# Performance work log

Hardware: AMD Instinct MI355X
Metric: run time of the kernel (lower is better)

Reference implementation:

```python
import jax, jax.numpy as jnp
import numpy as np

N, E, G = 50000, 800000, 64
IN_CH, HID, HEADS, NUM_CLASSES = 128, 64, 4, 10
NEG_SLOPE = 0.2


def _gat_conv(x, src, dst, W, a_src, a_dst, b, concat):
    """PyG-style GATConv with default add_self_loops=True (inference mode)."""
    n = x.shape[0]
    H, C = a_src.shape
    h = (x @ W).reshape(n, H, C)                       # [N,H,C]
    loop = jnp.arange(n, dtype=src.dtype)
    si = jnp.concatenate([src, loop])                  # [E+N]
    di = jnp.concatenate([dst, loop])
    as_n = jnp.sum(h * a_src, axis=-1)                 # [N,H]
    ad_n = jnp.sum(h * a_dst, axis=-1)                 # [N,H]
    e = jax.nn.leaky_relu(as_n[si] + ad_n[di], NEG_SLOPE)   # [E+N,H]
    m = jax.ops.segment_max(e, di, num_segments=n)     # segment softmax (stable)
    ex = jnp.exp(e - m[di])
    denom = jax.ops.segment_sum(ex, di, num_segments=n)
    alpha = ex / (denom[di] + 1e-16)                   # [E+N,H]
    out = jax.ops.segment_sum(alpha[:, :, None] * h[si], di, num_segments=n)  # [N,H,C]
    out = out.reshape(n, H * C) if concat else out.mean(axis=1)
    return out + b


def setup_inputs() -> dict:
    key = jax.random.key(0)
    ks = jax.random.split(key, 20)
    d = {}
    d["x"] = jax.random.normal(ks[0], (N, IN_CH), dtype=jnp.float32)
    d["src"] = jax.random.randint(ks[1], (E,), 0, N, dtype=jnp.int32)
    d["dst"] = jax.random.randint(ks[2], (E,), 0, N, dtype=jnp.int32)
    d["batch"] = jnp.sort(jax.random.randint(ks[3], (N,), 0, G, dtype=jnp.int32))
    s = 0.1
    d["W1"] = jax.random.normal(ks[4], (IN_CH, HEADS * HID), dtype=jnp.float32) * s
    d["as1"] = jax.random.normal(ks[5], (HEADS, HID), dtype=jnp.float32) * s
    d["ad1"] = jax.random.normal(ks[6], (HEADS, HID), dtype=jnp.float32) * s
    d["b1"] = jnp.zeros((HEADS * HID,), jnp.float32)
    d["W2"] = jax.random.normal(ks[7], (HEADS * HID, HEADS * HID), dtype=jnp.float32) * s
    d["as2"] = jax.random.normal(ks[8], (HEADS, HID), dtype=jnp.float32) * s
    d["ad2"] = jax.random.normal(ks[9], (HEADS, HID), dtype=jnp.float32) * s
    d["b2"] = jnp.zeros((HEADS * HID,), jnp.float32)
    # proj: 256 -> 64, heads=1, concat=False
    d["Wp"] = jax.random.normal(ks[10], (HEADS * HID, HID), dtype=jnp.float32) * s
    d["asp"] = jax.random.normal(ks[11], (1, HID), dtype=jnp.float32) * s
    d["adp"] = jax.random.normal(ks[12], (1, HID), dtype=jnp.float32) * s
    d["bp"] = jnp.zeros((HID,), jnp.float32)
    # MLP head
    d["Wh1"] = jax.random.normal(ks[13], (HID, HID), dtype=jnp.float32) * s
    d["bh1"] = jnp.zeros((HID,), jnp.float32)
    d["Wh2"] = jax.random.normal(ks[14], (HID, NUM_CLASSES), dtype=jnp.float32) * s
    d["bh2"] = jnp.zeros((NUM_CLASSES,), jnp.float32)
    return d


def reference(x, src, dst, batch, W1, as1, ad1, b1, W2, as2, ad2, b2,
              Wp, asp, adp, bp, Wh1, bh1, Wh2, bh2):
    h = jax.nn.elu(_gat_conv(x, src, dst, W1, as1, ad1, b1, concat=True))
    h = jax.nn.elu(_gat_conv(h, src, dst, W2, as2, ad2, b2, concat=True))
    h = jax.nn.elu(_gat_conv(h, src, dst, Wp, asp, adp, bp, concat=False))  # [N,HID]
    # global mean pool over graphs
    sums = jax.ops.segment_sum(h, batch, num_segments=G)                    # [G,HID]
    cnt = jax.ops.segment_sum(jnp.ones((h.shape[0],), h.dtype), batch, num_segments=G)
    g = sums / jnp.maximum(cnt, 1.0)[:, None]
    z = jax.nn.relu(g @ Wh1 + bh1)
    return z @ Wh2 + bh2                                                    # [G,NUM_CLASSES]
```

## Files before the change

### kernel.cpp

```cpp
#include <hip/hip_runtime.h>
#include <hip/hip_fp16.h>
#include <cstdint>
#include <cstddef>

#define NNODES 50000
#define NEDGES 800000
#define NGRAPH 64
#define BCAP 128

typedef __attribute__((ext_vector_type(8))) _Float16 half8;
typedef __attribute__((ext_vector_type(4))) float float4v;

__device__ __forceinline__ float lrelu(float x) { return x > 0.f ? x : 0.2f * x; }

__device__ __forceinline__ void wtrans_elem(const float* __restrict__ W,
                                            _Float16* __restrict__ Wt,
                                            int K, int N, int i) {
    int k = i / N, n = i - k * N;
    Wt[(size_t)n * K + k] = (_Float16)W[i];
}

__global__ void prep(const float* __restrict__ W1, const float* __restrict__ W2,
                     const float* __restrict__ Wp, _Float16* __restrict__ w1t,
                     _Float16* __restrict__ w2t, _Float16* __restrict__ wpt,
                     int* __restrict__ cnt) {
    int i = blockIdx.x * blockDim.x + threadIdx.x;
    if (i < 32768) wtrans_elem(W1, w1t, 128, 256, i);
    else if (i < 98304) wtrans_elem(W2, w2t, 256, 256, i - 32768);
    else if (i < 114688) wtrans_elem(Wp, wpt, 256, 64, i - 98304);
    else if (i < 114688 + NNODES) cnt[i - 114688] = 0;
}

__global__ __launch_bounds__(256) void scatter(const int* __restrict__ src,
                                               const int* __restrict__ dst,
                                               int* __restrict__ cnt,
                                               int* __restrict__ bucket) {
    int e = blockIdx.x * 256 + threadIdx.x;
    if (e < NEDGES) {
        int d = dst[e];
        int pos = atomicAdd(&cnt[d], 1);
        if (pos < BCAP) bucket[(size_t)d * BCAP + pos] = src[e];
    }
}

template <int KD, int NFB, int NTOT, int HTOT, bool F32A>
__global__ __launch_bounds__(256) void gemm_lds(const _Float16* __restrict__ A,
                                                const float* __restrict__ A32,
                                                const _Float16* __restrict__ Wt,
                                                const float* __restrict__ a_src,
                                                const float* __restrict__ a_dst,
                                                _Float16* __restrict__ C,
                                                float* __restrict__ as_n,
                                                float* __restrict__ ad_n,
                                                int M) {
    constexpr int NSPLIT = NTOT / (NFB * 16);
    constexpr int HLOC = NFB / 4;
    constexpr int KT = KD / 32;
    constexpr int KC = KD / 8;
    extern __shared__ _Float16 bsm[];

    const int bm = blockIdx.x / NSPLIT;
    const int bn = blockIdx.x % NSPLIT;
    const int tid = threadIdx.x;
    const int w = tid >> 6;
    const int lane = tid & 63;
    const int quad = lane >> 4;
    const int mcol = lane & 15;

    int arow = bm * 64 + w * 16 + mcol;
    if (arow >= M) arow = M - 1;

    half8 areg[KT];
    if constexpr (F32A) {
        const float* ap = A32 + (size_t)arow * KD + quad * 8;
        float4 t[KT * 2];
#pragma unroll
        for (int i = 0; i < KT; ++i) {
            t[2 * i]     = *reinterpret_cast<const float4*>(ap + i * 32);
            t[2 * i + 1] = *reinterpret_cast<const float4*>(ap + i * 32 + 4);
        }
#pragma unroll
        for (int i = 0; i < KT; ++i) {
            areg[i][0] = (_Float16)t[2 * i].x;     areg[i][1] = (_Float16)t[2 * i].y;
            areg[i][2] = (_Float16)t[2 * i].z;     areg[i][3] = (_Float16)t[2 * i].w;
            areg[i][4] = (_Float16)t[2 * i + 1].x; areg[i][5] = (_Float16)t[2 * i + 1].y;
            areg[i][6] = (_Float16)t[2 * i + 1].z; areg[i][7] = (_Float16)t[2 * i + 1].w;
        }
    } else {
        const _Float16* ap = A + (size_t)arow * KD + quad * 8;
#pragma unroll
        for (int i = 0; i < KT; ++i)
            areg[i] = *reinterpret_cast<const half8*>(ap + i * 32);
    }

    constexpr int CHUNKS = NFB * 16 * KC;
    const _Float16* wb = Wt + (size_t)bn * NFB * 16 * KD;
#pragma unroll
    for (int it = 0; it < CHUNKS / 256; ++it) {
        int idx = it * 256 + tid;
        int n = idx / KC, c = idx % KC;
        half8 v = *reinterpret_cast<const half8*>(wb + (size_t)n * KD + c * 8);
        *reinterpret_cast<half8*>(&bsm[n * KD + ((c ^ (n & 7)) * 8)]) = v;
    }
    __syncthreads();

    float4v acc[NFB];
#pragma unroll
    for (int nf = 0; nf < NFB; ++nf) acc[nf] = (float4v)0.f;
#pragma unroll
    for (int i = 0; i < KT; ++i) {
#pragma unroll
        for (int nf = 0; nf < NFB; ++nf) {
            int n = nf * 16 + mcol;
            int ch = (quad + i * 4) ^ (n & 7);
            half8 b = *reinterpret_cast<const half8*>(&bsm[n * KD + ch * 8]);
            acc[nf] = __builtin_amdgcn_mfma_f32_16x16x32_f16(areg[i], b, acc[nf], 0, 0, 0);
        }
    }

    const int orow0 = bm * 64 + w * 16 + quad * 4;
    const int cbase = bn * NFB * 16 + mcol;
#pragma unroll
    for (int r = 0; r < 4; ++r) {
        int orow = orow0 + r;
        if (orow < M) {
            _Float16* crow = C + (size_t)orow * NTOT + cbase;
#pragma unroll
            for (int nf = 0; nf < NFB; ++nf) crow[nf * 16] = (_Float16)acc[nf][r];
        }
    }

    float ps[HLOC][4], pd[HLOC][4];
#pragma unroll
    for (int hd = 0; hd < HLOC; ++hd)
#pragma unroll
        for (int r = 0; r < 4; ++r) { ps[hd][r] = 0.f; pd[hd][r] = 0.f; }
#pragma unroll
    for (int nf = 0; nf < NFB; ++nf) {
        float asv = a_src[bn * NFB * 16 + nf * 16 + mcol];
        float adv = a_dst[bn * NFB * 16 + nf * 16 + mcol];
#pragma unroll
        for (int r = 0; r < 4; ++r) {
            ps[nf >> 2][r] = fmaf(acc[nf][r], asv, ps[nf >> 2][r]);
            pd[nf >> 2][r] = fmaf(acc[nf][r], adv, pd[nf >> 2][r]);
        }
    }
#pragma unroll
    for (int off = 1; off < 16; off <<= 1) {
#pragma unroll
        for (int hd = 0; hd < HLOC; ++hd)
#pragma unroll
            for (int r = 0; r < 4; ++r) {
                ps[hd][r] += __shfl_xor(ps[hd][r], off);
                pd[hd][r] += __shfl_xor(pd[hd][r], off);
            }
    }
    if (mcol == 0) {
#pragma unroll
        for (int r = 0; r < 4; ++r) {
            int orow = orow0 + r;
            if (orow < M) {
#pragma unroll
                for (int hd = 0; hd < HLOC; ++hd) {
                    as_n[orow * HTOT + bn * HLOC + hd] = ps[hd][r];
                    ad_n[orow * HTOT + bn * HLOC + hd] = pd[hd][r];
                }
            }
        }
    }
}

template <int H, bool HALF_OUT>
__global__ __launch_bounds__(256) void node_agg(const int* __restrict__ bucket,
                                                const int* __restrict__ cnt,
                                                const __half* __restrict__ h,
                                                const float* __restrict__ asn,
                                                const float* __restrict__ adn,
                                                const float* __restrict__ bias,
                                                void* __restrict__ outv, int Nn) {
    constexpr int HC = H * 64;
    constexpr int VPL = HC / 64;
    constexpr int EPC = 64 / H;
    int n = blockIdx.x * 4 + (threadIdx.x >> 6);
    if (n >= Nn) return;
    const int lane = threadIdx.x & 63;
    const int hd = (H == 4) ? (lane >> 4) : 0;
    const int ej = (H == 4) ? (lane & 15) : lane;
    const int base = (H == 4) ? (lane & 48) : 0;
    const int rs = n * BCAP;
    const int re = rs + min(cnt[n], BCAP);

    const float ad = adn[n * H + hd];
    const float es = lrelu(asn[n * H + hd] + ad);

    float m = es;
    float denp = (ej == 0) ? 1.f : 0.f;
    float acc0, acc1, acc2, acc3;
    if (VPL == 4) {
        uint2 u = *reinterpret_cast<const uint2*>(&h[(size_t)n * HC + lane * 4]);
        float2 f0 = __half22float2(*reinterpret_cast<__half2*>(&u.x));
        float2 f1 = __half22float2(*reinterpret_cast<__half2*>(&u.y));
        acc0 = f0.x; acc1 = f0.y; acc2 = f1.x; acc3 = f1.y;
    } else {
        acc0 = __half2float(h[(size_t)n * HC + lane]);
        acc1 = acc2 = acc3 = 0.f;
    }

    auto body = [&](int j, float e, int s) {
        float ex = __shfl(e, base + j);
        int sj = __shfl(s, base + j);
        if (VPL == 4) {
            uint2 u = *reinterpret_cast<const uint2*>(&h[(size_t)sj * HC + lane * 4]);
            float2 f0 = __half22float2(*reinterpret_cast<__half2*>(&u.x));
            float2 f1 = __half22float2(*reinterpret_cast<__half2*>(&u.y));
            acc0 = fmaf(ex, f0.x, acc0);
            acc1 = fmaf(ex, f0.y, acc1);
            acc2 = fmaf(ex, f1.x, acc2);
            acc3 = fmaf(ex, f1.y, acc3);
        } else {
            acc0 = fmaf(ex, __half2float(h[(size_t)sj * HC + lane]), acc0);
        }
    };

    for (int c = rs; c < re; c += EPC) {
        int i = c + ej;
        int s = 0;
        float e = -1e30f;
        if (i < re) {
            s = bucket[i];
            e = lrelu(asn[s * H + hd] + ad);
        }
        float cm = e;
#pragma unroll
        for (int off = 1; off < EPC; off <<= 1) cm = fmaxf(cm, __shfl_xor(cm, off));
        float mn = fmaxf(m, cm);
        float scale = __expf(m - mn);
        m = mn;
        denp *= scale;
        acc0 *= scale; acc1 *= scale; acc2 *= scale; acc3 *= scale;
        float ex = __expf(e - m);
        denp += ex;
        const int cnt2 = min(EPC, re - c);
        if constexpr (EPC == 16) {
            if (cnt2 == 16) {
#pragma unroll
                for (int j = 0; j < 16; ++j) body(j, ex, s);
            } else {
                for (int j = 0; j < cnt2; ++j) body(j, ex, s);
            }
        } else {
#pragma unroll 8
            for (int j = 0; j < cnt2; ++j) body(j, ex, s);
        }
    }
    float den = denp;
#pragma unroll
    for (int off = 1; off < EPC; off <<= 1) den += __shfl_xor(den, off);

    const float inv = 1.f / (den + 1e-16f);
    if (VPL == 4) {
        float v0 = acc0 * inv + bias[lane * 4 + 0];
        float v1 = acc1 * inv + bias[lane * 4 + 1];
        float v2 = acc2 * inv + bias[lane * 4 + 2];
        float v3 = acc3 * inv + bias[lane * 4 + 3];
        v0 = v0 > 0.f ? v0 : expm1f(v0);
        v1 = v1 > 0.f ? v1 : expm1f(v1);
        v2 = v2 > 0.f ? v2 : expm1f(v2);
        v3 = v3 > 0.f ? v3 : expm1f(v3);
        if constexpr (HALF_OUT) {
            union { _Float16 h4[4]; uint2 u; } r;
            r.h4[0] = (_Float16)v0; r.h4[1] = (_Float16)v1;
            r.h4[2] = (_Float16)v2; r.h4[3] = (_Float16)v3;
            reinterpret_cast<uint2*>((_Float16*)outv + (size_t)n * HC)[lane] = r.u;
        } else {
            float4 o = make_float4(v0, v1, v2, v3);
            *reinterpret_cast<float4*>((float*)outv + (size_t)n * HC + lane * 4) = o;
        }
    } else {
        float v = acc0 * inv + bias[lane];
        v = v > 0.f ? v : expm1f(v);
        if constexpr (HALF_OUT)
            ((_Float16*)outv)[(size_t)n * HC + lane] = (_Float16)v;
        else
            ((float*)outv)[(size_t)n * HC + lane] = v;
    }
}

__global__ __launch_bounds__(256) void node_agg2(const int* __restrict__ bucket,
                                                 const int* __restrict__ cnt,
                                                 const __half* __restrict__ h,
                                                 const float* __restrict__ asn,
                                                 const float* __restrict__ adn,
                                                 const float* __restrict__ bias,
                                                 _Float16* __restrict__ outp, int Nn) {
    constexpr int H = 4, HC = 256, EPC = 16;
    const int wid = blockIdx.x * 4 + (threadIdx.x >> 6);
    int n0 = wid * 2;
    if (n0 >= Nn) return;
    int n1 = n0 + 1;
    const bool has1 = (n1 < Nn);
    if (!has1) n1 = n0;
    const int lane = threadIdx.x & 63;
    const int hd = lane >> 4;
    const int ej = lane & 15;
    const int base = lane & 48;
    const int rs0 = n0 * BCAP, rs1 = n1 * BCAP;
    const int re0 = rs0 + min(cnt[n0], BCAP);
    const int re1 = rs1 + min(cnt[n1], BCAP);

    const float ad0 = adn[n0 * H + hd];
    const float ad1 = adn[n1 * H + hd];
    const float es0 = lrelu(asn[n0 * H + hd] + ad0);
    const float es1 = lrelu(asn[n1 * H + hd] + ad1);

    float m0 = es0, m1 = es1;
    float dp0 = (ej == 0) ? 1.f : 0.f;
    float dp1 = dp0;

    float a0, a1, a2, a3, b0, b1, b2, b3;
    {
        uint2 u = *reinterpret_cast<const uint2*>(&h[(size_t)n0 * HC + lane * 4]);
        float2 f0 = __half22float2(*reinterpret_cast<__half2*>(&u.x));
        float2 f1 = __half22float2(*reinterpret_cast<__half2*>(&u.y));
        a0 = f0.x; a1 = f0.y; a2 = f1.x; a3 = f1.y;
    }
    {
        uint2 u = *reinterpret_cast<const uint2*>(&h[(size_t)n1 * HC + lane * 4]);
        float2 f0 = __half22float2(*reinterpret_cast<__half2*>(&u.x));
        float2 f1 = __half22float2(*reinterpret_cast<__half2*>(&u.y));
        b0 = f0.x; b1 = f0.y; b2 = f1.x; b3 = f1.y;
    }

    int c0 = rs0, c1 = rs1;
    while (c0 < re0 || c1 < re1) {
        const int i0 = c0 + ej, i1 = c1 + ej;
        int s0v = 0, s1v = 0;
        float e0 = -1e30f, e1 = -1e30f;
        if (i0 < re0) s0v = bucket[i0];
        if (i1 < re1) s1v = bucket[i1];
        if (i0 < re0) e0 = lrelu(asn[s0v * H + hd] + ad0);
        if (i1 < re1) e1 = lrelu(asn[s1v * H + hd] + ad1);

        float cm0 = e0, cm1 = e1;
#pragma unroll
        for (int off = 1; off < EPC; off <<= 1) {
            cm0 = fmaxf(cm0, __shfl_xor(cm0, off));
            cm1 = fmaxf(cm1, __shfl_xor(cm1, off));
        }
        const float mn0 = fmaxf(m0, cm0);
        const float mn1 = fmaxf(m1, cm1);
        const float sc0 = __expf(m0 - mn0);
        const float sc1 = __expf(m1 - mn1);
        m0 = mn0; m1 = mn1;
        dp0 *= sc0; dp1 *= sc1;
        a0 *= sc0; a1 *= sc0; a2 *= sc0; a3 *= sc0;
        b0 *= sc1; b1 *= sc1; b2 *= sc1; b3 *= sc1;
        const float x0 = __expf(e0 - m0);
        const float x1 = __expf(e1 - m1);
        dp0 += x0; dp1 += x1;

        auto bodyA = [&](int j) {
            float ex = __shfl(x0, base + j);
            int sj = __shfl(s0v, base + j);
            uint2 u = *reinterpret_cast<const uint2*>(&h[(size_t)sj * HC + lane * 4]);
            float2 f0 = __half22float2(*reinterpret_cast<__half2*>(&u.x));
            float2 f1 = __half22float2(*reinterpret_cast<__half2*>(&u.y));
            a0 = fmaf(ex, f0.x, a0);
            a1 = fmaf(ex, f0.y, a1);
            a2 = fmaf(ex, f1.x, a2);
            a3 = fmaf(ex, f1.y, a3);
        };
        auto bodyB = [&](int j) {
            float ex = __shfl(x1, base + j);
            int sj = __shfl(s1v, base + j);
            uint2 u = *reinterpret_cast<const uint2*>(&h[(size_t)sj * HC + lane * 4]);
            float2 f0 = __half22float2(*reinterpret_cast<__half2*>(&u.x));
            float2 f1 = __half22float2(*reinterpret_cast<__half2*>(&u.y));
            b0 = fmaf(ex, f0.x, b0);
            b1 = fmaf(ex, f0.y, b1);
            b2 = fmaf(ex, f1.x, b2);
            b3 = fmaf(ex, f1.y, b3);
        };

        const int nA = min(EPC, re0 - c0);
        const int nB = min(EPC, re1 - c1);
        const int nmax = max(nA, nB);
        if (nmax == EPC) {
#pragma unroll
            for (int j = 0; j < EPC; ++j) { bodyA(j); bodyB(j); }
        } else {
#pragma unroll 4
            for (int j = 0; j < nmax; ++j) { bodyA(j); bodyB(j); }
        }
        c0 += EPC; c1 += EPC;
    }

#pragma unroll
    for (int off = 1; off < EPC; off <<= 1) {
        dp0 += __shfl_xor(dp0, off);
        dp1 += __shfl_xor(dp1, off);
    }
    const float inv0 = 1.f / (dp0 + 1e-16f);
    const float inv1 = 1.f / (dp1 + 1e-16f);

    {
        float v0 = a0 * inv0 + bias[lane * 4 + 0];
        float v1 = a1 * inv0 + bias[lane * 4 + 1];
        float v2 = a2 * inv0 + bias[lane * 4 + 2];
        float v3 = a3 * inv0 + bias[lane * 4 + 3];
        v0 = v0 > 0.f ? v0 : expm1f(v0);
        v1 = v1 > 0.f ? v1 : expm1f(v1);
        v2 = v2 > 0.f ? v2 : expm1f(v2);
        v3 = v3 > 0.f ? v3 : expm1f(v3);
        union { _Float16 h4[4]; uint2 u; } r;
        r.h4[0] = (_Float16)v0; r.h4[1] = (_Float16)v1;
        r.h4[2] = (_Float16)v2; r.h4[3] = (_Float16)v3;
        reinterpret_cast<uint2*>(outp + (size_t)n0 * HC)[lane] = r.u;
    }
    if (has1) {
        float v0 = b0 * inv1 + bias[lane * 4 + 0];
        float v1 = b1 * inv1 + bias[lane * 4 + 1];
        float v2 = b2 * inv1 + bias[lane * 4 + 2];
        float v3 = b3 * inv1 + bias[lane * 4 + 3];
        v0 = v0 > 0.f ? v0 : expm1f(v0);
        v1 = v1 > 0.f ? v1 : expm1f(v1);
        v2 = v2 > 0.f ? v2 : expm1f(v2);
        v3 = v3 > 0.f ? v3 : expm1f(v3);
        union { _Float16 h4[4]; uint2 u; } r;
        r.h4[0] = (_Float16)v0; r.h4[1] = (_Float16)v1;
        r.h4[2] = (_Float16)v2; r.h4[3] = (_Float16)v3;
        reinterpret_cast<uint2*>(outp + (size_t)n1 * HC)[lane] = r.u;
    }
}

__global__ __launch_bounds__(256) void pool_mlp(const __half* __restrict__ feat,
                                                const int* __restrict__ batch,
                                                const float* __restrict__ Wh1,
                                                const float* __restrict__ bh1,
                                                const float* __restrict__ Wh2,
                                                const float* __restrict__ bh2,
                                                float* __restrict__ out, int Nn) {
    __shared__ float swsum[4][64];
    __shared__ float smean[64];
    __shared__ float shid[64];
    const int g = blockIdx.x;
    const int tid = threadIdx.x;
    const int lane = tid & 63;
    const int w = tid >> 6;
    int lo = 0, hi = Nn;
    while (lo < hi) { int mid = (lo + hi) >> 1; if (batch[mid] < g) lo = mid + 1; else hi = mid; }
    const int start = lo;
    hi = Nn;
    while (lo < hi) { int mid = (lo + hi) >> 1; if (batch[mid] < g + 1) lo = mid + 1; else hi = mid; }
    const int end = lo;
    float acc = 0.f;
    for (int n = start + w; n < end; n += 4) acc += __half2float(feat[(size_t)n * 64 + lane]);
    swsum[w][lane] = acc;
    __syncthreads();
    if (w == 0) {
        float s = swsum[0][lane] + swsum[1][lane] + swsum[2][lane] + swsum[3][lane];
        float c = (float)(end - start);
        c = c > 1.f ? c : 1.f;
        smean[lane] = s / c;
    }
    __syncthreads();
    if (tid < 64) {
        float a = bh1[tid];
        for (int k = 0; k < 64; ++k) a = fmaf(smean[k], Wh1[k * 64 + tid], a);
        shid[tid] = a > 0.f ? a : 0.f;
    }
    __syncthreads();
    if (tid < 10) {
        float a = bh2[tid];
        for (int k = 0; k < 64; ++k) a = fmaf(shid[k], Wh2[k * 10 + tid], a);
        out[g * 10 + tid] = a;
    }
}

extern "C" void kernel_launch(void* const* d_in, const int* in_sizes, int n_in,
                              void* d_out, int out_size, void* d_ws, size_t ws_size,
                              hipStream_t stream) {
    const float* x   = (const float*)d_in[0];
    const int* src   = (const int*)d_in[1];
    const int* dst   = (const int*)d_in[2];
    const int* batch = (const int*)d_in[3];
    const float* W1  = (const float*)d_in[4];
    const float* as1 = (const float*)d_in[5];
    const float* ad1 = (const float*)d_in[6];
    const float* b1  = (const float*)d_in[7];
    const float* W2  = (const float*)d_in[8];
    const float* as2 = (const float*)d_in[9];
    const float* ad2 = (const float*)d_in[10];
    const float* b2  = (const float*)d_in[11];
    const float* Wp  = (const float*)d_in[12];
    const float* asp = (const float*)d_in[13];
    const float* adp = (const float*)d_in[14];
    const float* bp  = (const float*)d_in[15];
    const float* Wh1 = (const float*)d_in[16];
    const float* bh1 = (const float*)d_in[17];
    const float* Wh2 = (const float*)d_in[18];
    const float* bh2 = (const float*)d_in[19];
    float* out = (float*)d_out;

    _Float16* hbase = (_Float16*)d_ws;
    const size_t NHC = (size_t)NNODES * 256;
    _Float16* ha16  = hbase;
    _Float16* hb16  = ha16 + NHC;
    _Float16* projh = hb16 + NHC;
    _Float16* w1t   = projh + (size_t)NNODES * 64;
    _Float16* w2t   = w1t + 256 * 128;
    _Float16* wpt   = w2t + 256 * 256;
    float* asn = (float*)(wpt + 64 * 256);
    float* adn = asn + (size_t)NNODES * 4;
    int* cnt    = (int*)(adn + (size_t)NNODES * 4);
    int* bucket = cnt + NNODES;

    const int gemmGrid = (NNODES + 63) / 64;
    const int scatGrid = (NEDGES + 255) / 256;
    const int agg2Grid = ((NNODES + 1) / 2 + 3) / 4;

    prep<<<(114688 + NNODES + 255) / 256, 256, 0, stream>>>(W1, W2, Wp, w1t, w2t, wpt, cnt);
    scatter<<<scatGrid, 256, 0, stream>>>(src, dst, cnt, bucket);
    gemm_lds<128, 8, 256, 4, true><<<gemmGrid * 2, 256, 32768, stream>>>(
        nullptr, x, w1t, as1, ad1, ha16, asn, adn, NNODES);
    node_agg2<<<agg2Grid, 256, 0, stream>>>(bucket, cnt,
        (const __half*)ha16, asn, adn, b1, hb16, NNODES);
    gemm_lds<256, 8, 256, 4, false><<<gemmGrid * 2, 256, 65536, stream>>>(
        hb16, nullptr, w2t, as2, ad2, ha16, asn, adn, NNODES);
    node_agg2<<<agg2Grid, 256, 0, stream>>>(bucket, cnt,
        (const __half*)ha16, asn, adn, b2, hb16, NNODES);
    gemm_lds<256, 4, 64, 1, false><<<gemmGrid, 256, 32768, stream>>>(
        hb16, nullptr, wpt, asp, adp, ha16, asn, adn, NNODES);
    node_agg<1, true><<<(NNODES + 3) / 4, 256, 0, stream>>>(bucket, cnt,
        (const __half*)ha16, asn, adn, bp, projh, NNODES);
    pool_mlp<<<NGRAPH, 256, 0, stream>>>((const __half*)projh, batch, Wh1, bh1, Wh2, bh2, out, NNODES);
}
```

Baseline: 478.7 us.

## Store node features in channel-sliced layout and aggregate per slice

GEMM outputs are written in a sliced layout ([slice][node][32 or 16 channels]) instead of row-major, and the next GEMM and the pooling kernel read that layout. The aggregation kernels are replaced by one templated kernel where each block handles one channel slice for a group of nodes. A wave covers several destination nodes with small lane groups, so each gathered neighbor read is a compact 64-byte (or 32-byte) segment and the per-slice working set is smaller and more cache-friendly. In exchange, each block recomputes the softmax weights for its slice, and the GEMM stores become strided scatters.

```diff
diff --git a/kernel.cpp b/kernel.cpp
--- a/kernel.cpp
+++ b/kernel.cpp
@@ -43,7 +43,7 @@
     }
 }
 
-template <int KD, int NFB, int NTOT, int HTOT, bool F32A>
+template <int KD, int NFB, int NTOT, int HTOT, bool F32A, int ISCH, int OSCH>
 __global__ __launch_bounds__(256) void gemm_lds(const _Float16* __restrict__ A,
                                                 const float* __restrict__ A32,
                                                 const _Float16* __restrict__ Wt,
@@ -54,7 +54,7 @@
                                                 float* __restrict__ ad_n,
                                                 int M) {
     constexpr int NSPLIT = NTOT / (NFB * 16);
-    constexpr int HLOC = NFB / 4;
+    constexpr int HLOC = (HTOT + NSPLIT - 1) / NSPLIT;
     constexpr int KT = KD / 32;
     constexpr int KC = KD / 8;
     extern __shared__ _Float16 bsm[];
@@ -86,6 +86,13 @@
             areg[i][4] = (_Float16)t[2 * i + 1].x; areg[i][5] = (_Float16)t[2 * i + 1].y;
             areg[i][6] = (_Float16)t[2 * i + 1].z; areg[i][7] = (_Float16)t[2 * i + 1].w;
         }
+    } else if constexpr (ISCH > 0) {
+#pragma unroll
+        for (int i = 0; i < KT; ++i) {
+            const int c0 = i * 32 + quad * 8;
+            areg[i] = *reinterpret_cast<const half8*>(
+                A + ((size_t)(c0 / ISCH) * M + arow) * ISCH + (c0 % ISCH));
+        }
     } else {
         const _Float16* ap = A + (size_t)arow * KD + quad * 8;
 #pragma unroll
@@ -119,14 +126,19 @@
     }
 
     const int orow0 = bm * 64 + w * 16 + quad * 4;
-    const int cbase = bn * NFB * 16 + mcol;
 #pragma unroll
     for (int r = 0; r < 4; ++r) {
         int orow = orow0 + r;
         if (orow < M) {
-            _Float16* crow = C + (size_t)orow * NTOT + cbase;
-#pragma unroll
-            for (int nf = 0; nf < NFB; ++nf) crow[nf * 16] = (_Float16)acc[nf][r];
+#pragma unroll
+            for (int nf = 0; nf < NFB; ++nf) {
+                const int col = bn * NFB * 16 + nf * 16 + mcol;
+                if constexpr (OSCH > 0)
+                    C[((size_t)(col / OSCH) * M + orow) * OSCH + (col % OSCH)] =
+                        (_Float16)acc[nf][r];
+                else
+                    C[(size_t)orow * NTOT + col] = (_Float16)acc[nf][r];
+            }
         }
     }
 
@@ -170,270 +182,102 @@
     }
 }
 
-template <int H, bool HALF_OUT>
-__global__ __launch_bounds__(256) void node_agg(const int* __restrict__ bucket,
-                                                const int* __restrict__ cnt,
-                                                const __half* __restrict__ h,
-                                                const float* __restrict__ asn,
-                                                const float* __restrict__ adn,
-                                                const float* __restrict__ bias,
-                                                void* __restrict__ outv, int Nn) {
-    constexpr int HC = H * 64;
-    constexpr int VPL = HC / 64;
-    constexpr int EPC = 64 / H;
-    int n = blockIdx.x * 4 + (threadIdx.x >> 6);
+template <int SLICES, int SCH, int HTOT>
+__global__ __launch_bounds__(256) void node_agg_s(const int* __restrict__ bucket,
+                                                  const int* __restrict__ cnt,
+                                                  const __half* __restrict__ hs,
+                                                  const float* __restrict__ asn,
+                                                  const float* __restrict__ adn,
+                                                  const float* __restrict__ bias,
+                                                  _Float16* __restrict__ outs,
+                                                  int Nn) {
+    constexpr int GL = SCH / 4;
+    constexpr int NPW = 64 / GL;
+    constexpr int HW = SLICES * SCH / HTOT;
+    const int s = blockIdx.x % SLICES;
+    const int nb = blockIdx.x / SLICES;
+    const int wv = threadIdx.x >> 6;
+    const int lane = threadIdx.x & 63;
+    const int li = lane % GL;
+    const int g = lane / GL;
+    const int n = nb * (4 * NPW) + wv * NPW + g;
     if (n >= Nn) return;
-    const int lane = threadIdx.x & 63;
-    const int hd = (H == 4) ? (lane >> 4) : 0;
-    const int ej = (H == 4) ? (lane & 15) : lane;
-    const int base = (H == 4) ? (lane & 48) : 0;
+    const int hd = (HTOT == 1) ? 0 : (s * SCH) / HW;
+    const int gb = lane - li;
+    const __half* __restrict__ hsl = hs + (size_t)s * Nn * SCH;
+    _Float16* __restrict__ osl = outs + (size_t)s * Nn * SCH;
+
     const int rs = n * BCAP;
     const int re = rs + min(cnt[n], BCAP);
-
-    const float ad = adn[n * H + hd];
-    const float es = lrelu(asn[n * H + hd] + ad);
-
-    float m = es;
-    float denp = (ej == 0) ? 1.f : 0.f;
-    float acc0, acc1, acc2, acc3;
-    if (VPL == 4) {
-        uint2 u = *reinterpret_cast<const uint2*>(&h[(size_t)n * HC + lane * 4]);
-        float2 f0 = __half22float2(*reinterpret_cast<__half2*>(&u.x));
-        float2 f1 = __half22float2(*reinterpret_cast<__half2*>(&u.y));
-        acc0 = f0.x; acc1 = f0.y; acc2 = f1.x; acc3 = f1.y;
-    } else {
-        acc0 = __half2float(h[(size_t)n * HC + lane]);
-        acc1 = acc2 = acc3 = 0.f;
-    }
-
-    auto body = [&](int j, float e, int s) {
-        float ex = __shfl(e, base + j);
-        int sj = __shfl(s, base + j);
-        if (VPL == 4) {
-            uint2 u = *reinterpret_cast<const uint2*>(&h[(size_t)sj * HC + lane * 4]);
-            float2 f0 = __half22float2(*reinterpret_cast<__half2*>(&u.x));
-            float2 f1 = __half22float2(*reinterpret_cast<__half2*>(&u.y));
-            acc0 = fmaf(ex, f0.x, acc0);
-            acc1 = fmaf(ex, f0.y, acc1);
-            acc2 = fmaf(ex, f1.x, acc2);
-            acc3 = fmaf(ex, f1.y, acc3);
-        } else {
-            acc0 = fmaf(ex, __half2float(h[(size_t)sj * HC + lane]), acc0);
-        }
-    };
-
-    for (int c = rs; c < re; c += EPC) {
-        int i = c + ej;
-        int s = 0;
-        float e = -1e30f;
-        if (i < re) {
-            s = bucket[i];
-            e = lrelu(asn[s * H + hd] + ad);
-        }
-        float cm = e;
-#pragma unroll
-        for (int off = 1; off < EPC; off <<= 1) cm = fmaxf(cm, __shfl_xor(cm, off));
-        float mn = fmaxf(m, cm);
-        float scale = __expf(m - mn);
-        m = mn;
-        denp *= scale;
-        acc0 *= scale; acc1 *= scale; acc2 *= scale; acc3 *= scale;
-        float ex = __expf(e - m);
-        denp += ex;
-        const int cnt2 = min(EPC, re - c);
-        if constexpr (EPC == 16) {
-            if (cnt2 == 16) {
-#pragma unroll
-                for (int j = 0; j < 16; ++j) body(j, ex, s);
-            } else {
-                for (int j = 0; j < cnt2; ++j) body(j, ex, s);
-            }
-        } else {
-#pragma unroll 8
-            for (int j = 0; j < cnt2; ++j) body(j, ex, s);
-        }
-    }
-    float den = denp;
-#pragma unroll
-    for (int off = 1; off < EPC; off <<= 1) den += __shfl_xor(den, off);
-
-    const float inv = 1.f / (den + 1e-16f);
-    if (VPL == 4) {
-        float v0 = acc0 * inv + bias[lane * 4 + 0];
-        float v1 = acc1 * inv + bias[lane * 4 + 1];
-        float v2 = acc2 * inv + bias[lane * 4 + 2];
-        float v3 = acc3 * inv + bias[lane * 4 + 3];
-        v0 = v0 > 0.f ? v0 : expm1f(v0);
-        v1 = v1 > 0.f ? v1 : expm1f(v1);
-        v2 = v2 > 0.f ? v2 : expm1f(v2);
-        v3 = v3 > 0.f ? v3 : expm1f(v3);
-        if constexpr (HALF_OUT) {
-            union { _Float16 h4[4]; uint2 u; } r;
-            r.h4[0] = (_Float16)v0; r.h4[1] = (_Float16)v1;
-            r.h4[2] = (_Float16)v2; r.h4[3] = (_Float16)v3;
-            reinterpret_cast<uint2*>((_Float16*)outv + (size_t)n * HC)[lane] = r.u;
-        } else {
-            float4 o = make_float4(v0, v1, v2, v3);
-            *reinterpret_cast<float4*>((float*)outv + (size_t)n * HC + lane * 4) = o;
-        }
-    } else {
-        float v = acc0 * inv + bias[lane];
-        v = v > 0.f ? v : expm1f(v);
-        if constexpr (HALF_OUT)
-            ((_Float16*)outv)[(size_t)n * HC + lane] = (_Float16)v;
-        else
-            ((float*)outv)[(size_t)n * HC + lane] = v;
-    }
-}
-
-__global__ __launch_bounds__(256) void node_agg2(const int* __restrict__ bucket,
-                                                 const int* __restrict__ cnt,
-                                                 const __half* __restrict__ h,
-                                                 const float* __restrict__ asn,
-                                                 const float* __restrict__ adn,
-                                                 const float* __restrict__ bias,
-                                                 _Float16* __restrict__ outp, int Nn) {
-    constexpr int H = 4, HC = 256, EPC = 16;
-    const int wid = blockIdx.x * 4 + (threadIdx.x >> 6);
-    int n0 = wid * 2;
-    if (n0 >= Nn) return;
-    int n1 = n0 + 1;
-    const bool has1 = (n1 < Nn);
-    if (!has1) n1 = n0;
-    const int lane = threadIdx.x & 63;
-    const int hd = lane >> 4;
-    const int ej = lane & 15;
-    const int base = lane & 48;
-    const int rs0 = n0 * BCAP, rs1 = n1 * BCAP;
-    const int re0 = rs0 + min(cnt[n0], BCAP);
-    const int re1 = rs1 + min(cnt[n1], BCAP);
-
-    const float ad0 = adn[n0 * H + hd];
-    const float ad1 = adn[n1 * H + hd];
-    const float es0 = lrelu(asn[n0 * H + hd] + ad0);
-    const float es1 = lrelu(asn[n1 * H + hd] + ad1);
-
-    float m0 = es0, m1 = es1;
-    float dp0 = (ej == 0) ? 1.f : 0.f;
-    float dp1 = dp0;
-
-    float a0, a1, a2, a3, b0, b1, b2, b3;
+    const float ad = adn[n * HTOT + hd];
+    float m = lrelu(asn[n * HTOT + hd] + ad);
+    float dp = (li == 0) ? 1.f : 0.f;
+
+    float a0, a1, a2, a3;
     {
-        uint2 u = *reinterpret_cast<const uint2*>(&h[(size_t)n0 * HC + lane * 4]);
+        uint2 u = *reinterpret_cast<const uint2*>(&hsl[(size_t)n * SCH + li * 4]);
         float2 f0 = __half22float2(*reinterpret_cast<__half2*>(&u.x));
         float2 f1 = __half22float2(*reinterpret_cast<__half2*>(&u.y));
         a0 = f0.x; a1 = f0.y; a2 = f1.x; a3 = f1.y;
     }
-    {
-        uint2 u = *reinterpret_cast<const uint2*>(&h[(size_t)n1 * HC + lane * 4]);
+
+    auto body = [&](int j, float x, int sv) {
+        float ex = __shfl(x, gb + j);
+        int sj = __shfl(sv, gb + j);
+        uint2 u = *reinterpret_cast<const uint2*>(&hsl[(size_t)sj * SCH + li * 4]);
         float2 f0 = __half22float2(*reinterpret_cast<__half2*>(&u.x));
         float2 f1 = __half22float2(*reinterpret_cast<__half2*>(&u.y));
-        b0 = f0.x; b1 = f0.y; b2 = f1.x; b3 = f1.y;
-    }
-
-    int c0 = rs0, c1 = rs1;
-    while (c0 < re0 || c1 < re1) {
-        const int i0 = c0 + ej, i1 = c1 + ej;
-        int s0v = 0, s1v = 0;
-        float e0 = -1e30f, e1 = -1e30f;
-        if (i0 < re0) s0v = bucket[i0];
-        if (i1 < re1) s1v = bucket[i1];
-        if (i0 < re0) e0 = lrelu(asn[s0v * H + hd] + ad0);
-        if (i1 < re1) e1 = lrelu(asn[s1v * H + hd] + ad1);
-
-        float cm0 = e0, cm1 = e1;
-#pragma unroll
-        for (int off = 1; off < EPC; off <<= 1) {
-            cm0 = fmaxf(cm0, __shfl_xor(cm0, off));
-            cm1 = fmaxf(cm1, __shfl_xor(cm1, off));
-        }
-        const float mn0 = fmaxf(m0, cm0);
-        const float mn1 = fmaxf(m1, cm1);
-        const float sc0 = __expf(m0 - mn0);
-        const float sc1 = __expf(m1 - mn1);
-        m0 = mn0; m1 = mn1;
-        dp0 *= sc0; dp1 *= sc1;
-        a0 *= sc0; a1 *= sc0; a2 *= sc0; a3 *= sc0;
-        b0 *= sc1; b1 *= sc1; b2 *= sc1; b3 *= sc1;
-        const float x0 = __expf(e0 - m0);
-        const float x1 = __expf(e1 - m1);
-        dp0 += x0; dp1 += x1;
-
-        auto bodyA = [&](int j) {
-            float ex = __shfl(x0, base + j);
-            int sj = __shfl(s0v, base + j);
-            uint2 u = *reinterpret_cast<const uint2*>(&h[(size_t)sj * HC + lane * 4]);
-            float2 f0 = __half22float2(*reinterpret_cast<__half2*>(&u.x));
-            float2 f1 = __half22float2(*reinterpret_cast<__half2*>(&u.y));
-            a0 = fmaf(ex, f0.x, a0);
-            a1 = fmaf(ex, f0.y, a1);
-            a2 = fmaf(ex, f1.x, a2);
-            a3 = fmaf(ex, f1.y, a3);
-        };
-        auto bodyB = [&](int j) {
-            float ex = __shfl(x1, base + j);
-            int sj = __shfl(s1v, base + j);
-            uint2 u = *reinterpret_cast<const uint2*>(&h[(size_t)sj * HC + lane * 4]);
-            float2 f0 = __half22float2(*reinterpret_cast<__half2*>(&u.x));
-            float2 f1 = __half22float2(*reinterpret_cast<__half2*>(&u.y));
-            b0 = fmaf(ex, f0.x, b0);
-            b1 = fmaf(ex, f0.y, b1);
-            b2 = fmaf(ex, f1.x, b2);
-            b3 = fmaf(ex, f1.y, b3);
-        };
-
-        const int nA = min(EPC, re0 - c0);
-        const int nB = min(EPC, re1 - c1);
-        const int nmax = max(nA, nB);
-        if (nmax == EPC) {
-#pragma unroll
-            for (int j = 0; j < EPC; ++j) { bodyA(j); bodyB(j); }
+        a0 = fmaf(ex, f0.x, a0);
+        a1 = fmaf(ex, f0.y, a1);
+        a2 = fmaf(ex, f1.x, a2);
+        a3 = fmaf(ex, f1.y, a3);
+    };
+
+    for (int c = rs; c < re; c += GL) {
+        int i = c + li;
+        int sv = 0;
+        float e = -1e30f;
+        if (i < re) {
+            sv = bucket[i];
+            e = lrelu(asn[sv * HTOT + hd] + ad);
+        }
+        float cm = e;
+#pragma unroll
+        for (int off = 1; off < GL; off <<= 1) cm = fmaxf(cm, __shfl_xor(cm, off));
+        float mn = fmaxf(m, cm);
+        float sc = __expf(m - mn);
+        m = mn;
+        dp *= sc;
+        a0 *= sc; a1 *= sc; a2 *= sc; a3 *= sc;
+        float x = __expf(e - m);
+        dp += x;
+        const int nb2 = min(GL, re - c);
+        if (nb2 == GL) {
+#pragma unroll
+            for (int j = 0; j < GL; ++j) body(j, x, sv);
         } else {
-#pragma unroll 4
-            for (int j = 0; j < nmax; ++j) { bodyA(j); bodyB(j); }
-        }
-        c0 += EPC; c1 += EPC;
-    }
-
-#pragma unroll
-    for (int off = 1; off < EPC; off <<= 1) {
-        dp0 += __shfl_xor(dp0, off);
-        dp1 += __shfl_xor(dp1, off);
-    }
-    const float inv0 = 1.f / (dp0 + 1e-16f);
-    const float inv1 = 1.f / (dp1 + 1e-16f);
-
-    {
-        float v0 = a0 * inv0 + bias[lane * 4 + 0];
-        float v1 = a1 * inv0 + bias[lane * 4 + 1];
-        float v2 = a2 * inv0 + bias[lane * 4 + 2];
-        float v3 = a3 * inv0 + bias[lane * 4 + 3];
-        v0 = v0 > 0.f ? v0 : expm1f(v0);
-        v1 = v1 > 0.f ? v1 : expm1f(v1);
-        v2 = v2 > 0.f ? v2 : expm1f(v2);
-        v3 = v3 > 0.f ? v3 : expm1f(v3);
-        union { _Float16 h4[4]; uint2 u; } r;
-        r.h4[0] = (_Float16)v0; r.h4[1] = (_Float16)v1;
-        r.h4[2] = (_Float16)v2; r.h4[3] = (_Float16)v3;
-        reinterpret_cast<uint2*>(outp + (size_t)n0 * HC)[lane] = r.u;
-    }
-    if (has1) {
-        float v0 = b0 * inv1 + bias[lane * 4 + 0];
-        float v1 = b1 * inv1 + bias[lane * 4 + 1];
-        float v2 = b2 * inv1 + bias[lane * 4 + 2];
-        float v3 = b3 * inv1 + bias[lane * 4 + 3];
-        v0 = v0 > 0.f ? v0 : expm1f(v0);
-        v1 = v1 > 0.f ? v1 : expm1f(v1);
-        v2 = v2 > 0.f ? v2 : expm1f(v2);
-        v3 = v3 > 0.f ? v3 : expm1f(v3);
-        union { _Float16 h4[4]; uint2 u; } r;
-        r.h4[0] = (_Float16)v0; r.h4[1] = (_Float16)v1;
-        r.h4[2] = (_Float16)v2; r.h4[3] = (_Float16)v3;
-        reinterpret_cast<uint2*>(outp + (size_t)n1 * HC)[lane] = r.u;
-    }
-}
-
-__global__ __launch_bounds__(256) void pool_mlp(const __half* __restrict__ feat,
+            for (int j = 0; j < nb2; ++j) body(j, x, sv);
+        }
+    }
+#pragma unroll
+    for (int off = 1; off < GL; off <<= 1) dp += __shfl_xor(dp, off);
+    const float inv = 1.f / (dp + 1e-16f);
+    const int cb = s * SCH + li * 4;
+    float v0 = a0 * inv + bias[cb + 0];
+    float v1 = a1 * inv + bias[cb + 1];
+    float v2 = a2 * inv + bias[cb + 2];
+    float v3 = a3 * inv + bias[cb + 3];
+    v0 = v0 > 0.f ? v0 : expm1f(v0);
+    v1 = v1 > 0.f ? v1 : expm1f(v1);
+    v2 = v2 > 0.f ? v2 : expm1f(v2);
+    v3 = v3 > 0.f ? v3 : expm1f(v3);
+    union { _Float16 h4[4]; uint2 u; } r;
+    r.h4[0] = (_Float16)v0; r.h4[1] = (_Float16)v1;
+    r.h4[2] = (_Float16)v2; r.h4[3] = (_Float16)v3;
+    *reinterpret_cast<uint2*>(&osl[(size_t)n * SCH + li * 4]) = r.u;
+}
+
+__global__ __launch_bounds__(256) void pool_mlp(const _Float16* __restrict__ feat,
                                                 const int* __restrict__ batch,
                                                 const float* __restrict__ Wh1,
                                                 const float* __restrict__ bh1,
@@ -453,8 +297,9 @@
     hi = Nn;
     while (lo < hi) { int mid = (lo + hi) >> 1; if (batch[mid] < g + 1) lo = mid + 1; else hi = mid; }
     const int end = lo;
+    const _Float16* fp = feat + (size_t)(lane >> 4) * Nn * 16 + (lane & 15);
     float acc = 0.f;
-    for (int n = start + w; n < end; n += 4) acc += __half2float(feat[(size_t)n * 64 + lane]);
+    for (int n = start + w; n < end; n += 4) acc += (float)fp[(size_t)n * 16];
     swsum[w][lane] = acc;
     __syncthreads();
     if (w == 0) {
@@ -517,21 +362,22 @@
 
     const int gemmGrid = (NNODES + 63) / 64;
     const int scatGrid = (NEDGES + 255) / 256;
-    const int agg2Grid = ((NNODES + 1) / 2 + 3) / 4;
+    const int agg4Grid = 8 * ((NNODES + 31) / 32);
+    const int aggPGrid = 4 * ((NNODES + 63) / 64);
 
     prep<<<(114688 + NNODES + 255) / 256, 256, 0, stream>>>(W1, W2, Wp, w1t, w2t, wpt, cnt);
     scatter<<<scatGrid, 256, 0, stream>>>(src, dst, cnt, bucket);
-    gemm_lds<128, 8, 256, 4, true><<<gemmGrid * 2, 256, 32768, stream>>>(
+    gemm_lds<128, 8, 256, 4, true, 0, 32><<<gemmGrid * 2, 256, 32768, stream>>>(
         nullptr, x, w1t, as1, ad1, ha16, asn, adn, NNODES);
-    node_agg2<<<agg2Grid, 256, 0, stream>>>(bucket, cnt,
+    node_agg_s<8, 32, 4><<<agg4Grid, 256, 0, stream>>>(bucket, cnt,
         (const __half*)ha16, asn, adn, b1, hb16, NNODES);
-    gemm_lds<256, 8, 256, 4, false><<<gemmGrid * 2, 256, 65536, stream>>>(
+    gemm_lds<256, 8, 256, 4, false, 32, 32><<<gemmGrid * 2, 256, 65536, stream>>>(
         hb16, nullptr, w2t, as2, ad2, ha16, asn, adn, NNODES);
-    node_agg2<<<agg2Grid, 256, 0, stream>>>(bucket, cnt,
+    node_agg_s<8, 32, 4><<<agg4Grid, 256, 0, stream>>>(bucket, cnt,
         (const __half*)ha16, asn, adn, b2, hb16, NNODES);
-    gemm_lds<256, 4, 64, 1, false><<<gemmGrid, 256, 32768, stream>>>(
+    gemm_lds<256, 4, 64, 1, false, 32, 16><<<gemmGrid, 256, 32768, stream>>>(
         hb16, nullptr, wpt, asp, adp, ha16, asn, adn, NNODES);
-    node_agg<1, true><<<(NNODES + 3) / 4, 256, 0, stream>>>(bucket, cnt,
+    node_agg_s<4, 16, 1><<<aggPGrid, 256, 0, stream>>>(bucket, cnt,
         (const __half*)ha16, asn, adn, bp, projh, NNODES);
-    pool_mlp<<<NGRAPH, 256, 0, stream>>>((const __half*)projh, batch, Wh1, bh1, Wh2, bh2, out, NNODES);
-}
+    pool_mlp<<<NGRAPH, 256, 0, stream>>>(projh, batch, Wh1, bh1, Wh2, bh2, out, NNODES);
+}
```

After: 559.7 us. 1.17x slower.
